# Optimization experiments

Hardware: AMD Instinct MI355X
Metric: run time of the kernel (lower is better)

Reference implementation:

```python
import jax, jax.numpy as jnp
import numpy as np

N, IN_C, OUT_C, H, CF = 4096, 256, 256, 8, 6
D = OUT_C // H

def setup_inputs() -> dict:
    key = jax.random.key(0)
    ks = jax.random.split(key, 8)
    x = jax.random.normal(ks[0], (N, IN_C), dtype=jnp.float32)
    positions = jax.random.normal(ks[1], (N, 3), dtype=jnp.float32)
    curv_feats = jax.random.normal(ks[2], (N, CF), dtype=jnp.float32)
    adj = jax.random.randint(ks[3], (N, N), 0, 2, dtype=jnp.int32)
    W = jax.random.normal(ks[4], (OUT_C, IN_C), dtype=jnp.float32) * 0.05
    a_l = jax.random.normal(ks[5], (H, D), dtype=jnp.float32) * 0.1
    a_r = jax.random.normal(ks[6], (H, D), dtype=jnp.float32) * 0.1
    Wc = jax.random.normal(ks[7], (H, CF), dtype=jnp.float32) * 0.1
    gate = jnp.asarray(0.1, dtype=jnp.float32)
    return {"x": x, "positions": positions, "curv_feats": curv_feats,
            "adj": adj, "W": W, "a_l": a_l, "a_r": a_r, "Wc": Wc, "gate": gate}

def reference(x, positions, curv_feats, adj, W, a_l, a_r, Wc, gate):
    n = x.shape[0]
    h = (x @ W.T).reshape(n, H, D)                       # (N,H,D)
    e_l = jnp.einsum('nhd,hd->nh', h, a_l)               # (N,H)
    e_r = jnp.einsum('nhd,hd->nh', h, a_r)               # (N,H)
    logits = jax.nn.leaky_relu(e_l[:, None, :] + e_r[None, :, :], negative_slope=0.2)  # (N,N,H)
    curv_pair = jnp.abs(curv_feats[:, None, :] - curv_feats[None, :, :])  # (N,N,CF)
    curv_bias = jnp.einsum('ijf,hf->ijh', curv_pair, Wc)                  # (N,N,H)
    logits = logits + gate * curv_bias
    mask = (adj > 0)[:, :, None]                          # (N,N,1)
    logits = jnp.where(mask, logits, jnp.float32(-1e9))
    attn = jax.nn.softmax(logits, axis=1)                 # softmax over j (dim=1)
    out = jnp.einsum('ijh,jhd->ihd', attn, h)             # (N,H,D)
    return out.reshape(n, H * D)
```

## Files before the change

kernel.cpp:

```cpp
#include <hip/hip_runtime.h>

#define NN 4096
#define HC 8
#define DC 32
#define OC 256
#define KC 256
#define CF 6

typedef __bf16 bf16_t;
typedef bf16_t bf16x8 __attribute__((ext_vector_type(8)));
typedef float f32x4 __attribute__((ext_vector_type(4)));
typedef float f32x2 __attribute__((ext_vector_type(2)));
typedef unsigned u32x4 __attribute__((ext_vector_type(4)));

#if defined(__has_builtin)
#if __has_builtin(__builtin_amdgcn_exp2f)
#define EXP2F(x) __builtin_amdgcn_exp2f(x)
#else
#define EXP2F(x) exp2f(x)
#endif
#else
#define EXP2F(x) exp2f(x)
#endif

static __device__ __forceinline__ f32x2 unpk(unsigned dw) {
  union { unsigned u; float f; } lo, hi;
  lo.u = dw << 16;
  hi.u = dw & 0xffff0000u;
  return (f32x2){lo.f, hi.f};
}

__global__ __launch_bounds__(256) void prep_all(const float* __restrict__ x,
                                                const float* __restrict__ W,
                                                const float* __restrict__ a_l,
                                                const float* __restrict__ a_r,
                                                const int* __restrict__ adj,
                                                const float* __restrict__ cfeat,
                                                const float* __restrict__ Wc,
                                                const float* __restrict__ gate,
                                                float* __restrict__ e_l2,
                                                bf16_t* __restrict__ erP,
                                                bf16_t* __restrict__ hT2,
                                                unsigned* __restrict__ adjb,
                                                float* __restrict__ cfT,
                                                bf16_t* __restrict__ cfP,
                                                float* __restrict__ Wc2) {
  __shared__ float As[16][68];
  __shared__ float Bs[16][36];
  __shared__ float Ct[DC][65];
  const float LOG2E = 1.44269504088896340736f;
  const int t = threadIdx.x;
  const int bid = blockIdx.x;

  if (bid >= 512) {
    const int pb = bid - 512;
    const int ptid = pb * 256 + t;
    const int lane = t & 63;
    const int wv = pb * 4 + (t >> 6);
    for (int it = 0; it < 32; ++it) {
      int g = wv * 32 + it;
      int i = g >> 6;
      int s = g & 63;
      int v = adj[(size_t)i * NN + s * 64 + lane];
      unsigned long long m = __ballot(v > 0);
      if (lane == 0) *(unsigned long long*)(adjb + i * 128 + s * 2) = m;
    }
    if (ptid < NN * CF) {
      int j = ptid / CF, f = ptid - j * CF;
      float v = cfeat[ptid];
      cfT[f * NN + j] = v;
      int cc = j >> 5, qq = (j >> 3) & 3, tt = j & 7;
      cfP[((cc * 4 + qq) * CF + f) * 8 + tt] = (bf16_t)v;
    }
    if (ptid < HC * CF) Wc2[ptid] = Wc[ptid] * gate[0] * LOG2E;
    return;
  }

  const int i0 = (bid & 63) * 64;
  const int head = bid >> 6;
  const int c0 = head * DC;
  const int tx = t & 7;
  const int ty = t >> 3;
  const int lr = t >> 2;
  const int lk = (t & 3) * 4;

  float acc[2][4] = {};
  for (int kk = 0; kk < KC; kk += 16) {
    f32x4 av = *(const f32x4*)&x[(size_t)(i0 + lr) * KC + kk + lk];
    f32x4 wv;
    if (t < 128) wv = *(const f32x4*)&W[(size_t)(c0 + (t >> 2)) * KC + kk + lk];
    __syncthreads();
    As[lk + 0][lr] = av[0]; As[lk + 1][lr] = av[1];
    As[lk + 2][lr] = av[2]; As[lk + 3][lr] = av[3];
    if (t < 128) {
      int br = t >> 2;
      Bs[lk + 0][br] = wv[0]; Bs[lk + 1][br] = wv[1];
      Bs[lk + 2][br] = wv[2]; Bs[lk + 3][br] = wv[3];
    }
    __syncthreads();
#pragma unroll
    for (int k = 0; k < 16; ++k) {
      f32x2 a = *(const f32x2*)&As[k][ty * 2];
      f32x4 b = *(const f32x4*)&Bs[k][tx * 4];
#pragma unroll
      for (int r = 0; r < 2; ++r)
#pragma unroll
        for (int u = 0; u < 4; ++u)
          acc[r][u] += a[r] * b[u];
    }
  }

  f32x4 al4 = *(const f32x4*)&a_l[c0 + tx * 4];
  f32x4 ar4 = *(const f32x4*)&a_r[c0 + tx * 4];
#pragma unroll
  for (int r = 0; r < 2; ++r) {
    float el = acc[r][0] * al4[0] + acc[r][1] * al4[1] +
               acc[r][2] * al4[2] + acc[r][3] * al4[3];
    float er = acc[r][0] * ar4[0] + acc[r][1] * ar4[1] +
               acc[r][2] * ar4[2] + acc[r][3] * ar4[3];
    el += __shfl_xor(el, 1, 64); el += __shfl_xor(el, 2, 64); el += __shfl_xor(el, 4, 64);
    er += __shfl_xor(er, 1, 64); er += __shfl_xor(er, 2, 64); er += __shfl_xor(er, 4, 64);
    if (tx == 0) {
      int j = i0 + ty * 2 + r;
      e_l2[j * HC + head] = el * LOG2E;
      int cc = j >> 5, qq = (j >> 3) & 3, tt = j & 7;
      erP[((cc * 4 + qq) * HC + head) * 8 + tt] = (bf16_t)(er * LOG2E);
    }
  }

#pragma unroll
  for (int r = 0; r < 2; ++r)
#pragma unroll
    for (int u = 0; u < 4; ++u)
      Ct[tx * 4 + u][ty * 2 + r] = acc[r][u];
  __syncthreads();
  const size_t base = (size_t)head * (NN / 32) * 1024 + (size_t)(bid & 63) * 2048;
#pragma unroll
  for (int rep = 0; rep < 8; ++rep) {
    int idx = rep * 256 + t;
    int dd = (idx >> 3) & 31;
    int jl = (idx >> 10) * 32 + ((idx >> 8) & 3) * 8 + (idx & 7);
    hT2[base + idx] = (bf16_t)Ct[dd][jl];
  }
}

__global__ __launch_bounds__(256, 4) void attn(const unsigned* __restrict__ adjb,
                                               const float* __restrict__ e_l2,
                                               const float* __restrict__ cfT,
                                               const float* __restrict__ Wc2,
                                               const u32x4* __restrict__ cfP4,
                                               const u32x4* __restrict__ erP4,
                                               const bf16_t* __restrict__ hT2,
                                               float* __restrict__ out) {
  __shared__ float Obuf[16][64];
  __shared__ float Sbuf[16][2];
  const int tid = threadIdx.x;
  const int w = tid >> 6;
  const int lane = tid & 63;
  const int il = lane & 15;
  const int quad = lane >> 4;
  const int ibase = blockIdx.x * 16;
  const int hg = blockIdx.y;
  const int i = ibase + il;

  for (int idx = tid; idx < 16 * 64; idx += 256) (&Obuf[0][0])[idx] = 0.f;
  if (tid < 32) (&Sbuf[0][0])[tid] = 0.f;
  __syncthreads();

  f32x2 cfi2[CF];
#pragma unroll
  for (int f = 0; f < CF; ++f) { float v = cfT[f * NN + i]; cfi2[f] = (f32x2){v, v}; }
  f32x2 el2[2];
  {
    f32x2 e0 = *(const f32x2*)&e_l2[i * HC + hg * 2];
#pragma unroll
    for (int u = 0; u < 2; ++u) el2[u] = (f32x2){e0[u], e0[u]};
  }
  float wc[2][CF];
#pragma unroll
  for (int h = 0; h < 2; ++h)
#pragma unroll
    for (int f = 0; f < CF; ++f) wc[h][f] = Wc2[(hg * 2 + h) * CF + f];

  f32x4 acc[2][2];
#pragma unroll
  for (int h = 0; h < 2; ++h)
#pragma unroll
    for (int d = 0; d < 2; ++d) acc[h][d] = (f32x4){0.f, 0.f, 0.f, 0.f};
  f32x2 S2[2];
#pragma unroll
  for (int h = 0; h < 2; ++h) S2[h] = (f32x2){0.f, 0.f};

  const bf16_t* hTbase = hT2 + (size_t)hg * 2 * ((NN / 32) * 1024) + quad * 256 + il * 8;
  const u32x4* cfb = cfP4 + quad * CF;
  const u32x4* erb = erP4 + quad * HC + hg * 2;
  const unsigned* adjrow = adjb + i * 128;

  u32x4 cfc[CF];
#pragma unroll
  for (int f = 0; f < CF; ++f) cfc[f] = cfb[w * (4 * CF) + f];
  u32x4 erc[2];
#pragma unroll
  for (int h = 0; h < 2; ++h) erc[h] = erb[w * (4 * HC) + h];
  unsigned mc = adjrow[w];

#pragma unroll 2
  for (int c = w; c < NN / 32; c += 4) {
    const bf16_t* bp0 = hTbase + c * 1024;
    const bf16_t* bp1 = bp0 + (NN / 32) * 1024;
    bf16x8 b00 = *(const bf16x8*)bp0;
    bf16x8 b01 = *(const bf16x8*)(bp0 + 128);
    bf16x8 b10 = *(const bf16x8*)bp1;
    bf16x8 b11 = *(const bf16x8*)(bp1 + 128);

    f32x2 arg[2][4];
#pragma unroll
    for (int h = 0; h < 2; ++h)
#pragma unroll
      for (int p = 0; p < 4; ++p) {
        f32x2 s = el2[h] + unpk(erc[h][p]);
        arg[h][p] = __builtin_elementwise_max(s, 0.2f * s);
      }
#pragma unroll
    for (int f = 0; f < CF; ++f) {
#pragma unroll
      for (int p = 0; p < 4; ++p) {
        f32x2 d2 = cfi2[f] - unpk(cfc[f][p]);
        f32x2 ab = __builtin_elementwise_max(d2, -d2);
#pragma unroll
        for (int h = 0; h < 2; ++h) {
          f32x2 wsp = (f32x2){wc[h][f], wc[h][f]};
          arg[h][p] = __builtin_elementwise_fma(ab, wsp, arg[h][p]);
        }
      }
    }

    const int cn = (c + 4) & (NN / 32 - 1);
    const unsigned m8 = (mc >> (quad * 8)) & 0xffu;
#pragma unroll
    for (int f = 0; f < CF; ++f) cfc[f] = cfb[cn * (4 * CF) + f];
#pragma unroll
    for (int h = 0; h < 2; ++h) erc[h] = erb[cn * (4 * HC) + h];
    mc = adjrow[cn];

    f32x2 mf2[4];
#pragma unroll
    for (int p = 0; p < 4; ++p)
      mf2[p] = (f32x2){(float)((m8 >> (2 * p)) & 1u), (float)((m8 >> (2 * p + 1)) & 1u)};

#pragma unroll
    for (int h = 0; h < 2; ++h) {
      bf16x8 af;
#pragma unroll
      for (int p = 0; p < 4; ++p) {
        f32x2 pv = (f32x2){EXP2F(arg[h][p][0]), EXP2F(arg[h][p][1])};
        pv = pv * mf2[p];
        S2[h] += pv;
        af[2 * p] = (bf16_t)pv[0];
        af[2 * p + 1] = (bf16_t)pv[1];
      }
      acc[h][0] = __builtin_amdgcn_mfma_f32_16x16x32_bf16(af, h ? b10 : b00, acc[h][0], 0, 0, 0);
      acc[h][1] = __builtin_amdgcn_mfma_f32_16x16x32_bf16(af, h ? b11 : b01, acc[h][1], 0, 0, 0);
    }
  }

#pragma unroll
  for (int h = 0; h < 2; ++h) {
    float v = S2[h][0] + S2[h][1];
    v += __shfl_xor(v, 16, 64);
    v += __shfl_xor(v, 32, 64);
    if (quad == 0) atomicAdd(&Sbuf[il][h], v);
  }
#pragma unroll
  for (int h = 0; h < 2; ++h)
#pragma unroll
    for (int dh = 0; dh < 2; ++dh)
#pragma unroll
      for (int r = 0; r < 4; ++r)
        atomicAdd(&Obuf[quad * 4 + r][h * DC + dh * 16 + il], acc[h][dh][r]);
  __syncthreads();

  for (int idx = tid; idx < 16 * 64; idx += 256) {
    int row = idx >> 6;
    int colg = idx & 63;
    out[(size_t)(ibase + row) * OC + hg * 64 + colg] =
        Obuf[row][colg] / Sbuf[row][colg >> 5];
  }
}

extern "C" void kernel_launch(void* const* d_in, const int* in_sizes, int n_in,
                              void* d_out, int out_size, void* d_ws, size_t ws_size,
                              hipStream_t stream) {
  const float* x    = (const float*)d_in[0];
  const float* cfeat= (const float*)d_in[2];
  const int*   adj  = (const int*)d_in[3];
  const float* W    = (const float*)d_in[4];
  const float* a_l  = (const float*)d_in[5];
  const float* a_r  = (const float*)d_in[6];
  const float* Wc   = (const float*)d_in[7];
  const float* gate = (const float*)d_in[8];
  float* out = (float*)d_out;

  char* ws = (char*)d_ws;
  bf16_t*   hT2  = (bf16_t*)ws;
  unsigned* adjb = (unsigned*)(ws + (2u << 20));
  float*    e_l2 = (float*)(ws + (4u << 20));
  float*    cfT  = (float*)(ws + (4u << 20) + (128u << 10));
  float*    Wc2  = (float*)(ws + (4u << 20) + (256u << 10));
  bf16_t*   cfP  = (bf16_t*)(ws + (4u << 20) + (320u << 10));
  bf16_t*   erP  = (bf16_t*)(ws + (4u << 20) + (384u << 10));

  prep_all<<<2560, 256, 0, stream>>>(x, W, a_l, a_r, adj, cfeat, Wc, gate,
                                     e_l2, erP, hT2, adjb, cfT, cfP, Wc2);
  attn<<<dim3(NN / 16, 4), 256, 0, stream>>>(adjb, e_l2, cfT, Wc2,
                                             (const u32x4*)cfP, (const u32x4*)erP,
                                             hT2, out);
}
```

Measured before the change: 230.7 us.

## Process four heads per block with 512 threads to share curvature work

The attention kernel now handles four heads per block instead of two, and uses 8 waves of 512 threads across the j-chunks, with the grid's head dimension halved. The |cf_i - cf_j| terms and the mask are computed once per pair and reused across four heads, which cuts redundant VALU work in the curvature bias. The loop is also reordered so each pair's logits are built and exponentiated head by head, with the next chunk's prefetch moved inside. The cost is more registers (accumulators, B fragments and exponent arguments for four heads) and fewer blocks, which may lower occupancy or cause spills under launch_bounds(512,4).

```diff
diff --git a/kernel.cpp b/kernel.cpp
--- a/kernel.cpp
+++ b/kernel.cpp
@@ -144,7 +144,7 @@
   }
 }
 
-__global__ __launch_bounds__(256, 4) void attn(const unsigned* __restrict__ adjb,
+__global__ __launch_bounds__(512, 4) void attn(const unsigned* __restrict__ adjb,
                                                const float* __restrict__ e_l2,
                                                const float* __restrict__ cfT,
                                                const float* __restrict__ Wc2,
@@ -152,8 +152,8 @@
                                                const u32x4* __restrict__ erP4,
                                                const bf16_t* __restrict__ hT2,
                                                float* __restrict__ out) {
-  __shared__ float Obuf[16][64];
-  __shared__ float Sbuf[16][2];
+  __shared__ float Obuf[16][128];
+  __shared__ float Sbuf[16][4];
   const int tid = threadIdx.x;
   const int w = tid >> 6;
   const int lane = tid & 63;
@@ -162,117 +162,117 @@
   const int ibase = blockIdx.x * 16;
   const int hg = blockIdx.y;
   const int i = ibase + il;
-
-  for (int idx = tid; idx < 16 * 64; idx += 256) (&Obuf[0][0])[idx] = 0.f;
-  if (tid < 32) (&Sbuf[0][0])[tid] = 0.f;
+  const int HSTRIDE = (NN / 32) * 1024;
+
+  for (int idx = tid; idx < 16 * 128; idx += 512) (&Obuf[0][0])[idx] = 0.f;
+  if (tid < 64) (&Sbuf[0][0])[tid] = 0.f;
   __syncthreads();
 
   f32x2 cfi2[CF];
 #pragma unroll
   for (int f = 0; f < CF; ++f) { float v = cfT[f * NN + i]; cfi2[f] = (f32x2){v, v}; }
-  f32x2 el2[2];
+  f32x2 el2[4];
   {
-    f32x2 e0 = *(const f32x2*)&e_l2[i * HC + hg * 2];
-#pragma unroll
-    for (int u = 0; u < 2; ++u) el2[u] = (f32x2){e0[u], e0[u]};
-  }
-  float wc[2][CF];
-#pragma unroll
-  for (int h = 0; h < 2; ++h)
-#pragma unroll
-    for (int f = 0; f < CF; ++f) wc[h][f] = Wc2[(hg * 2 + h) * CF + f];
-
-  f32x4 acc[2][2];
-#pragma unroll
-  for (int h = 0; h < 2; ++h)
+    f32x4 e0 = *(const f32x4*)&e_l2[i * HC + hg * 4];
+#pragma unroll
+    for (int u = 0; u < 4; ++u) el2[u] = (f32x2){e0[u], e0[u]};
+  }
+  float wc[4][CF];
+#pragma unroll
+  for (int h = 0; h < 4; ++h)
+#pragma unroll
+    for (int f = 0; f < CF; ++f) wc[h][f] = Wc2[(hg * 4 + h) * CF + f];
+
+  f32x4 acc[4][2];
+#pragma unroll
+  for (int h = 0; h < 4; ++h)
 #pragma unroll
     for (int d = 0; d < 2; ++d) acc[h][d] = (f32x4){0.f, 0.f, 0.f, 0.f};
-  f32x2 S2[2];
-#pragma unroll
-  for (int h = 0; h < 2; ++h) S2[h] = (f32x2){0.f, 0.f};
-
-  const bf16_t* hTbase = hT2 + (size_t)hg * 2 * ((NN / 32) * 1024) + quad * 256 + il * 8;
+  f32x2 S2[4];
+#pragma unroll
+  for (int h = 0; h < 4; ++h) S2[h] = (f32x2){0.f, 0.f};
+
+  const bf16_t* hTbase = hT2 + (size_t)hg * 4 * HSTRIDE + quad * 256 + il * 8;
   const u32x4* cfb = cfP4 + quad * CF;
-  const u32x4* erb = erP4 + quad * HC + hg * 2;
+  const u32x4* erb = erP4 + quad * HC + hg * 4;
   const unsigned* adjrow = adjb + i * 128;
 
   u32x4 cfc[CF];
 #pragma unroll
   for (int f = 0; f < CF; ++f) cfc[f] = cfb[w * (4 * CF) + f];
-  u32x4 erc[2];
-#pragma unroll
-  for (int h = 0; h < 2; ++h) erc[h] = erb[w * (4 * HC) + h];
+  u32x4 erc[4];
+#pragma unroll
+  for (int h = 0; h < 4; ++h) erc[h] = erb[w * (4 * HC) + h];
   unsigned mc = adjrow[w];
 
 #pragma unroll 2
-  for (int c = w; c < NN / 32; c += 4) {
-    const bf16_t* bp0 = hTbase + c * 1024;
-    const bf16_t* bp1 = bp0 + (NN / 32) * 1024;
-    bf16x8 b00 = *(const bf16x8*)bp0;
-    bf16x8 b01 = *(const bf16x8*)(bp0 + 128);
-    bf16x8 b10 = *(const bf16x8*)bp1;
-    bf16x8 b11 = *(const bf16x8*)(bp1 + 128);
-
-    f32x2 arg[2][4];
-#pragma unroll
-    for (int h = 0; h < 2; ++h)
-#pragma unroll
-      for (int p = 0; p < 4; ++p) {
-        f32x2 s = el2[h] + unpk(erc[h][p]);
-        arg[h][p] = __builtin_elementwise_max(s, 0.2f * s);
+  for (int c = w; c < NN / 32; c += 8) {
+    const bf16_t* bp = hTbase + c * 1024;
+    bf16x8 bfr[4][2];
+#pragma unroll
+    for (int h = 0; h < 4; ++h) {
+      bfr[h][0] = *(const bf16x8*)(bp + h * HSTRIDE);
+      bfr[h][1] = *(const bf16x8*)(bp + h * HSTRIDE + 128);
+    }
+
+    const unsigned m8 = (mc >> (quad * 8)) & 0xffu;
+    bf16x8 af[4];
+
+#pragma unroll
+    for (int p = 0; p < 4; ++p) {
+      f32x2 ab[CF];
+#pragma unroll
+      for (int f = 0; f < CF; ++f) {
+        f32x2 d2 = cfi2[f] - unpk(cfc[f][p]);
+        ab[f] = __builtin_elementwise_max(d2, -d2);
       }
-#pragma unroll
-    for (int f = 0; f < CF; ++f) {
-#pragma unroll
-      for (int p = 0; p < 4; ++p) {
-        f32x2 d2 = cfi2[f] - unpk(cfc[f][p]);
-        f32x2 ab = __builtin_elementwise_max(d2, -d2);
-#pragma unroll
-        for (int h = 0; h < 2; ++h) {
+      f32x2 mf2 = (f32x2){(float)((m8 >> (2 * p)) & 1u),
+                          (float)((m8 >> (2 * p + 1)) & 1u)};
+      f32x2 sv[4];
+#pragma unroll
+      for (int h = 0; h < 4; ++h) sv[h] = el2[h] + unpk(erc[h][p]);
+
+      if (p == 3) {
+        const int cn = (c + 8) & (NN / 32 - 1);
+#pragma unroll
+        for (int f = 0; f < CF; ++f) cfc[f] = cfb[cn * (4 * CF) + f];
+#pragma unroll
+        for (int h = 0; h < 4; ++h) erc[h] = erb[cn * (4 * HC) + h];
+        mc = adjrow[cn];
+      }
+
+#pragma unroll
+      for (int h = 0; h < 4; ++h) {
+        f32x2 a = __builtin_elementwise_max(sv[h], 0.2f * sv[h]);
+#pragma unroll
+        for (int f = 0; f < CF; ++f) {
           f32x2 wsp = (f32x2){wc[h][f], wc[h][f]};
-          arg[h][p] = __builtin_elementwise_fma(ab, wsp, arg[h][p]);
+          a = __builtin_elementwise_fma(ab[f], wsp, a);
         }
+        f32x2 pv = (f32x2){EXP2F(a[0]), EXP2F(a[1])};
+        pv = pv * mf2;
+        S2[h] += pv;
+        af[h][2 * p] = (bf16_t)pv[0];
+        af[h][2 * p + 1] = (bf16_t)pv[1];
       }
     }
 
-    const int cn = (c + 4) & (NN / 32 - 1);
-    const unsigned m8 = (mc >> (quad * 8)) & 0xffu;
-#pragma unroll
-    for (int f = 0; f < CF; ++f) cfc[f] = cfb[cn * (4 * CF) + f];
-#pragma unroll
-    for (int h = 0; h < 2; ++h) erc[h] = erb[cn * (4 * HC) + h];
-    mc = adjrow[cn];
-
-    f32x2 mf2[4];
-#pragma unroll
-    for (int p = 0; p < 4; ++p)
-      mf2[p] = (f32x2){(float)((m8 >> (2 * p)) & 1u), (float)((m8 >> (2 * p + 1)) & 1u)};
-
-#pragma unroll
-    for (int h = 0; h < 2; ++h) {
-      bf16x8 af;
-#pragma unroll
-      for (int p = 0; p < 4; ++p) {
-        f32x2 pv = (f32x2){EXP2F(arg[h][p][0]), EXP2F(arg[h][p][1])};
-        pv = pv * mf2[p];
-        S2[h] += pv;
-        af[2 * p] = (bf16_t)pv[0];
-        af[2 * p + 1] = (bf16_t)pv[1];
-      }
-      acc[h][0] = __builtin_amdgcn_mfma_f32_16x16x32_bf16(af, h ? b10 : b00, acc[h][0], 0, 0, 0);
-      acc[h][1] = __builtin_amdgcn_mfma_f32_16x16x32_bf16(af, h ? b11 : b01, acc[h][1], 0, 0, 0);
-    }
-  }
-
-#pragma unroll
-  for (int h = 0; h < 2; ++h) {
+#pragma unroll
+    for (int h = 0; h < 4; ++h) {
+      acc[h][0] = __builtin_amdgcn_mfma_f32_16x16x32_bf16(af[h], bfr[h][0], acc[h][0], 0, 0, 0);
+      acc[h][1] = __builtin_amdgcn_mfma_f32_16x16x32_bf16(af[h], bfr[h][1], acc[h][1], 0, 0, 0);
+    }
+  }
+
+#pragma unroll
+  for (int h = 0; h < 4; ++h) {
     float v = S2[h][0] + S2[h][1];
     v += __shfl_xor(v, 16, 64);
     v += __shfl_xor(v, 32, 64);
     if (quad == 0) atomicAdd(&Sbuf[il][h], v);
   }
 #pragma unroll
-  for (int h = 0; h < 2; ++h)
+  for (int h = 0; h < 4; ++h)
 #pragma unroll
     for (int dh = 0; dh < 2; ++dh)
 #pragma unroll
@@ -280,10 +280,10 @@
         atomicAdd(&Obuf[quad * 4 + r][h * DC + dh * 16 + il], acc[h][dh][r]);
   __syncthreads();
 
-  for (int idx = tid; idx < 16 * 64; idx += 256) {
-    int row = idx >> 6;
-    int colg = idx & 63;
-    out[(size_t)(ibase + row) * OC + hg * 64 + colg] =
+  for (int idx = tid; idx < 16 * 128; idx += 512) {
+    int row = idx >> 7;
+    int colg = idx & 127;
+    out[(size_t)(ibase + row) * OC + hg * 128 + colg] =
         Obuf[row][colg] / Sbuf[row][colg >> 5];
   }
 }
@@ -312,7 +312,7 @@
 
   prep_all<<<2560, 256, 0, stream>>>(x, W, a_l, a_r, adj, cfeat, Wc, gate,
                                      e_l2, erP, hT2, adjb, cfT, cfP, Wc2);
-  attn<<<dim3(NN / 16, 4), 256, 0, stream>>>(adjb, e_l2, cfT, Wc2,
+  attn<<<dim3(NN / 16, 2), 512, 0, stream>>>(adjb, e_l2, cfT, Wc2,
                                              (const u32x4*)cfP, (const u32x4*)erP,
                                              hT2, out);
 }
```

New measurement: 334.1 us. +44.8%, slower.

## Switch attention logits to packed fp16 math and fp16 MFMA, prefetch prep loads

Applied to the files above, without the earlier changes.

Stores h, e_r and curvature features as fp16 instead of bf16 and computes the leaky-relu logits and curvature bias with packed half-precision arithmetic. This halves the VALU work of the inner pairwise loop. The exp results are packed with cvt_pkrtz and fed to the fp16 MFMA, and masked entries skip the exp entirely through a select. The prep kernel also batches the adjacency loads ahead of the ballots and software-prefetches the next x/W tile in the GEMM. In exchange, fp16 logits carry less precision and range, and unmasked logits could overflow exp2 in fp16 packing.

```diff
diff --git a/kernel.cpp b/kernel.cpp
--- a/kernel.cpp
+++ b/kernel.cpp
@@ -7,8 +7,10 @@
 #define KC 256
 #define CF 6
 
-typedef __bf16 bf16_t;
-typedef bf16_t bf16x8 __attribute__((ext_vector_type(8)));
+typedef _Float16 f16_t;
+typedef f16_t f16x2 __attribute__((ext_vector_type(2)));
+typedef f16_t f16x8 __attribute__((ext_vector_type(8)));
+typedef __fp16 hh2 __attribute__((ext_vector_type(2)));
 typedef float f32x4 __attribute__((ext_vector_type(4)));
 typedef float f32x2 __attribute__((ext_vector_type(2)));
 typedef unsigned u32x4 __attribute__((ext_vector_type(4)));
@@ -23,12 +25,7 @@
 #define EXP2F(x) exp2f(x)
 #endif
 
-static __device__ __forceinline__ f32x2 unpk(unsigned dw) {
-  union { unsigned u; float f; } lo, hi;
-  lo.u = dw << 16;
-  hi.u = dw & 0xffff0000u;
-  return (f32x2){lo.f, hi.f};
-}
+union HU { f16x2 h; unsigned u; };
 
 __global__ __launch_bounds__(256) void prep_all(const float* __restrict__ x,
                                                 const float* __restrict__ W,
@@ -39,11 +36,11 @@
                                                 const float* __restrict__ Wc,
                                                 const float* __restrict__ gate,
                                                 float* __restrict__ e_l2,
-                                                bf16_t* __restrict__ erP,
-                                                bf16_t* __restrict__ hT2,
+                                                f16_t* __restrict__ erP,
+                                                f16_t* __restrict__ hT2,
                                                 unsigned* __restrict__ adjb,
                                                 float* __restrict__ cfT,
-                                                bf16_t* __restrict__ cfP,
+                                                f16_t* __restrict__ cfP,
                                                 float* __restrict__ Wc2) {
   __shared__ float As[16][68];
   __shared__ float Bs[16][36];
@@ -57,20 +54,24 @@
     const int ptid = pb * 256 + t;
     const int lane = t & 63;
     const int wv = pb * 4 + (t >> 6);
-    for (int it = 0; it < 32; ++it) {
-      int g = wv * 32 + it;
-      int i = g >> 6;
-      int s = g & 63;
-      int v = adj[(size_t)i * NN + s * 64 + lane];
-      unsigned long long m = __ballot(v > 0);
-      if (lane == 0) *(unsigned long long*)(adjb + i * 128 + s * 2) = m;
+    int v[32];
+#pragma unroll
+    for (int u = 0; u < 32; ++u) {
+      int g = wv * 32 + u;
+      v[u] = adj[(size_t)(g >> 6) * NN + (g & 63) * 64 + lane];
+    }
+#pragma unroll
+    for (int u = 0; u < 32; ++u) {
+      int g = wv * 32 + u;
+      unsigned long long m = __ballot(v[u] > 0);
+      if (lane == 0) *(unsigned long long*)(adjb + (g >> 6) * 128 + (g & 63) * 2) = m;
     }
     if (ptid < NN * CF) {
       int j = ptid / CF, f = ptid - j * CF;
-      float v = cfeat[ptid];
-      cfT[f * NN + j] = v;
+      float vv = cfeat[ptid];
+      cfT[f * NN + j] = vv;
       int cc = j >> 5, qq = (j >> 3) & 3, tt = j & 7;
-      cfP[((cc * 4 + qq) * CF + f) * 8 + tt] = (bf16_t)v;
+      cfP[((cc * 4 + qq) * CF + f) * 8 + tt] = (f16_t)vv;
     }
     if (ptid < HC * CF) Wc2[ptid] = Wc[ptid] * gate[0] * LOG2E;
     return;
@@ -85,10 +86,10 @@
   const int lk = (t & 3) * 4;
 
   float acc[2][4] = {};
+  f32x4 av = *(const f32x4*)&x[(size_t)(i0 + lr) * KC + lk];
+  f32x4 wv = {};
+  if (t < 128) wv = *(const f32x4*)&W[(size_t)(c0 + (t >> 2)) * KC + lk];
   for (int kk = 0; kk < KC; kk += 16) {
-    f32x4 av = *(const f32x4*)&x[(size_t)(i0 + lr) * KC + kk + lk];
-    f32x4 wv;
-    if (t < 128) wv = *(const f32x4*)&W[(size_t)(c0 + (t >> 2)) * KC + kk + lk];
     __syncthreads();
     As[lk + 0][lr] = av[0]; As[lk + 1][lr] = av[1];
     As[lk + 2][lr] = av[2]; As[lk + 3][lr] = av[3];
@@ -98,6 +99,10 @@
       Bs[lk + 2][br] = wv[2]; Bs[lk + 3][br] = wv[3];
     }
     __syncthreads();
+    if (kk + 16 < KC) {
+      av = *(const f32x4*)&x[(size_t)(i0 + lr) * KC + kk + 16 + lk];
+      if (t < 128) wv = *(const f32x4*)&W[(size_t)(c0 + (t >> 2)) * KC + kk + 16 + lk];
+    }
 #pragma unroll
     for (int k = 0; k < 16; ++k) {
       f32x2 a = *(const f32x2*)&As[k][ty * 2];
@@ -124,7 +129,7 @@
       int j = i0 + ty * 2 + r;
       e_l2[j * HC + head] = el * LOG2E;
       int cc = j >> 5, qq = (j >> 3) & 3, tt = j & 7;
-      erP[((cc * 4 + qq) * HC + head) * 8 + tt] = (bf16_t)(er * LOG2E);
+      erP[((cc * 4 + qq) * HC + head) * 8 + tt] = (f16_t)(er * LOG2E);
     }
   }
 
@@ -140,7 +145,7 @@
     int idx = rep * 256 + t;
     int dd = (idx >> 3) & 31;
     int jl = (idx >> 10) * 32 + ((idx >> 8) & 3) * 8 + (idx & 7);
-    hT2[base + idx] = (bf16_t)Ct[dd][jl];
+    hT2[base + idx] = (f16_t)Ct[dd][jl];
   }
 }
 
@@ -150,7 +155,7 @@
                                                const float* __restrict__ Wc2,
                                                const u32x4* __restrict__ cfP4,
                                                const u32x4* __restrict__ erP4,
-                                               const bf16_t* __restrict__ hT2,
+                                               const f16_t* __restrict__ hT2,
                                                float* __restrict__ out) {
   __shared__ float Obuf[16][64];
   __shared__ float Sbuf[16][2];
@@ -167,31 +172,36 @@
   if (tid < 32) (&Sbuf[0][0])[tid] = 0.f;
   __syncthreads();
 
-  f32x2 cfi2[CF];
-#pragma unroll
-  for (int f = 0; f < CF; ++f) { float v = cfT[f * NN + i]; cfi2[f] = (f32x2){v, v}; }
-  f32x2 el2[2];
+  f16x2 cfi2h[CF];
+#pragma unroll
+  for (int f = 0; f < CF; ++f) {
+    f16_t v = (f16_t)cfT[f * NN + i];
+    cfi2h[f] = (f16x2){v, v};
+  }
+  f16x2 elh[2];
   {
     f32x2 e0 = *(const f32x2*)&e_l2[i * HC + hg * 2];
 #pragma unroll
-    for (int u = 0; u < 2; ++u) el2[u] = (f32x2){e0[u], e0[u]};
-  }
-  float wc[2][CF];
+    for (int u = 0; u < 2; ++u) { f16_t v = (f16_t)e0[u]; elh[u] = (f16x2){v, v}; }
+  }
+  f16x2 wch[2][CF];
 #pragma unroll
   for (int h = 0; h < 2; ++h)
 #pragma unroll
-    for (int f = 0; f < CF; ++f) wc[h][f] = Wc2[(hg * 2 + h) * CF + f];
+    for (int f = 0; f < CF; ++f) {
+      f16_t v = (f16_t)Wc2[(hg * 2 + h) * CF + f];
+      wch[h][f] = (f16x2){v, v};
+    }
+  const f16x2 lslope = (f16x2){(f16_t)0.2f, (f16_t)0.2f};
 
   f32x4 acc[2][2];
 #pragma unroll
   for (int h = 0; h < 2; ++h)
 #pragma unroll
     for (int d = 0; d < 2; ++d) acc[h][d] = (f32x4){0.f, 0.f, 0.f, 0.f};
-  f32x2 S2[2];
-#pragma unroll
-  for (int h = 0; h < 2; ++h) S2[h] = (f32x2){0.f, 0.f};
-
-  const bf16_t* hTbase = hT2 + (size_t)hg * 2 * ((NN / 32) * 1024) + quad * 256 + il * 8;
+  float S[2] = {0.f, 0.f};
+
+  const f16_t* hTbase = hT2 + (size_t)hg * 2 * ((NN / 32) * 1024) + quad * 256 + il * 8;
   const u32x4* cfb = cfP4 + quad * CF;
   const u32x4* erb = erP4 + quad * HC + hg * 2;
   const unsigned* adjrow = adjb + i * 128;
@@ -206,67 +216,73 @@
 
 #pragma unroll 2
   for (int c = w; c < NN / 32; c += 4) {
-    const bf16_t* bp0 = hTbase + c * 1024;
-    const bf16_t* bp1 = bp0 + (NN / 32) * 1024;
-    bf16x8 b00 = *(const bf16x8*)bp0;
-    bf16x8 b01 = *(const bf16x8*)(bp0 + 128);
-    bf16x8 b10 = *(const bf16x8*)bp1;
-    bf16x8 b11 = *(const bf16x8*)(bp1 + 128);
-
-    f32x2 arg[2][4];
-#pragma unroll
-    for (int h = 0; h < 2; ++h)
-#pragma unroll
-      for (int p = 0; p < 4; ++p) {
-        f32x2 s = el2[h] + unpk(erc[h][p]);
-        arg[h][p] = __builtin_elementwise_max(s, 0.2f * s);
+    const f16_t* bp0 = hTbase + c * 1024;
+    const f16_t* bp1 = bp0 + (NN / 32) * 1024;
+    f16x8 b00 = *(const f16x8*)bp0;
+    f16x8 b01 = *(const f16x8*)(bp0 + 128);
+    f16x8 b10 = *(const f16x8*)bp1;
+    f16x8 b11 = *(const f16x8*)(bp1 + 128);
+
+    f16x2 arg[2][4];
+#pragma unroll
+    for (int p = 0; p < 4; ++p) {
+      f16x2 bias0 = (f16x2){(f16_t)0.f, (f16_t)0.f};
+      f16x2 bias1 = (f16x2){(f16_t)0.f, (f16_t)0.f};
+#pragma unroll
+      for (int f = 0; f < CF; ++f) {
+        HU cu; cu.u = cfc[f][p];
+        f16x2 d = cfi2h[f] - cu.h;
+        f16x2 ad = __builtin_elementwise_max(d, -d);
+        bias0 = __builtin_elementwise_fma(ad, wch[0][f], bias0);
+        bias1 = __builtin_elementwise_fma(ad, wch[1][f], bias1);
       }
 #pragma unroll
-    for (int f = 0; f < CF; ++f) {
-#pragma unroll
-      for (int p = 0; p < 4; ++p) {
-        f32x2 d2 = cfi2[f] - unpk(cfc[f][p]);
-        f32x2 ab = __builtin_elementwise_max(d2, -d2);
-#pragma unroll
-        for (int h = 0; h < 2; ++h) {
-          f32x2 wsp = (f32x2){wc[h][f], wc[h][f]};
-          arg[h][p] = __builtin_elementwise_fma(ab, wsp, arg[h][p]);
-        }
+      for (int h = 0; h < 2; ++h) {
+        HU eu; eu.u = erc[h][p];
+        f16x2 s = elh[h] + eu.h;
+        f16x2 lk = __builtin_elementwise_max(s, lslope * s);
+        arg[h][p] = lk + (h ? bias1 : bias0);
       }
     }
-
-    const int cn = (c + 4) & (NN / 32 - 1);
     const unsigned m8 = (mc >> (quad * 8)) & 0xffu;
-#pragma unroll
-    for (int f = 0; f < CF; ++f) cfc[f] = cfb[cn * (4 * CF) + f];
-#pragma unroll
-    for (int h = 0; h < 2; ++h) erc[h] = erb[cn * (4 * HC) + h];
-    mc = adjrow[cn];
-
-    f32x2 mf2[4];
-#pragma unroll
-    for (int p = 0; p < 4; ++p)
-      mf2[p] = (f32x2){(float)((m8 >> (2 * p)) & 1u), (float)((m8 >> (2 * p + 1)) & 1u)};
+
+    {
+      const int cn = (c + 4) & (NN / 32 - 1);
+#pragma unroll
+      for (int f = 0; f < CF; ++f) cfc[f] = cfb[cn * (4 * CF) + f];
+#pragma unroll
+      for (int h = 0; h < 2; ++h) erc[h] = erb[cn * (4 * HC) + h];
+      mc = adjrow[cn];
+    }
+
+    union { f16x8 v; unsigned u[4]; } af[2];
+#pragma unroll
+    for (int p = 0; p < 4; ++p) {
+      const unsigned b0 = (m8 >> (2 * p)) & 1u;
+      const unsigned b1 = (m8 >> (2 * p + 1)) & 1u;
+#pragma unroll
+      for (int h = 0; h < 2; ++h) {
+        float lo = (float)arg[h][p][0];
+        float hi = (float)arg[h][p][1];
+        float e0 = b0 ? EXP2F(lo) : 0.f;
+        float e1 = b1 ? EXP2F(hi) : 0.f;
+        S[h] += e0 + e1;
+        union { hh2 r; unsigned u; } cv;
+        cv.r = __builtin_amdgcn_cvt_pkrtz(e0, e1);
+        af[h].u[p] = cv.u;
+      }
+    }
 
 #pragma unroll
     for (int h = 0; h < 2; ++h) {
-      bf16x8 af;
-#pragma unroll
-      for (int p = 0; p < 4; ++p) {
-        f32x2 pv = (f32x2){EXP2F(arg[h][p][0]), EXP2F(arg[h][p][1])};
-        pv = pv * mf2[p];
-        S2[h] += pv;
-        af[2 * p] = (bf16_t)pv[0];
-        af[2 * p + 1] = (bf16_t)pv[1];
-      }
-      acc[h][0] = __builtin_amdgcn_mfma_f32_16x16x32_bf16(af, h ? b10 : b00, acc[h][0], 0, 0, 0);
-      acc[h][1] = __builtin_amdgcn_mfma_f32_16x16x32_bf16(af, h ? b11 : b01, acc[h][1], 0, 0, 0);
+      acc[h][0] = __builtin_amdgcn_mfma_f32_16x16x32_f16(af[h].v, h ? b10 : b00, acc[h][0], 0, 0, 0);
+      acc[h][1] = __builtin_amdgcn_mfma_f32_16x16x32_f16(af[h].v, h ? b11 : b01, acc[h][1], 0, 0, 0);
     }
   }
 
 #pragma unroll
   for (int h = 0; h < 2; ++h) {
-    float v = S2[h][0] + S2[h][1];
+    float v = S[h];
     v += __shfl_xor(v, 16, 64);
     v += __shfl_xor(v, 32, 64);
     if (quad == 0) atomicAdd(&Sbuf[il][h], v);
@@ -302,13 +318,13 @@
   float* out = (float*)d_out;
 
   char* ws = (char*)d_ws;
-  bf16_t*   hT2  = (bf16_t*)ws;
+  f16_t*    hT2  = (f16_t*)ws;
   unsigned* adjb = (unsigned*)(ws + (2u << 20));
   float*    e_l2 = (float*)(ws + (4u << 20));
   float*    cfT  = (float*)(ws + (4u << 20) + (128u << 10));
   float*    Wc2  = (float*)(ws + (4u << 20) + (256u << 10));
-  bf16_t*   cfP  = (bf16_t*)(ws + (4u << 20) + (320u << 10));
-  bf16_t*   erP  = (bf16_t*)(ws + (4u << 20) + (384u << 10));
+  f16_t*    cfP  = (f16_t*)(ws + (4u << 20) + (320u << 10));
+  f16_t*    erP  = (f16_t*)(ws + (4u << 20) + (384u << 10));
 
   prep_all<<<2560, 256, 0, stream>>>(x, W, a_l, a_r, adj, cfeat, Wc, gate,
                                      e_l2, erP, hT2, adjb, cfT, cfP, Wc2);
```

Measured after the change: 187.5 us. 18.7% less time.
